# Kernel optimization log

Hardware: AMD Instinct MI355X
Metric: run time of the kernel (lower is better)

Reference implementation:

```python
import jax, jax.numpy as jnp
import numpy as np

B, M, V, D = 2048, 2, 25, 64      # batch, max_body, joints, input channels
C1, C2, K, U = 128, 256, 3, 256   # gcn hidden, gcn out, A kernel size, lstm units
NJ, NB = M * V * U, M * U         # joint / body state widths
SD = NJ + NB + U                  # full state dim = 13568


def _hs(z):
    # keras hard_sigmoid
    return jnp.clip(0.2 * z + 0.5, 0.0, 1.0)


def _lstm_step(z, c):
    i = _hs(z[..., :U])
    f = _hs(z[..., U:2 * U])
    g = jnp.tanh(z[..., 2 * U:3 * U])
    o = _hs(z[..., 3 * U:])
    c2 = f * c + i * g
    return o * jnp.tanh(c2), c2


def _forget_bias(shape_prefix):
    z = jnp.zeros(shape_prefix + (U,), jnp.float32)
    return jnp.concatenate([z, jnp.ones_like(z), z, z], axis=-1)


def setup_inputs() -> dict:
    key = jax.random.key(0)
    ks = jax.random.split(key, 16)
    f = lambda i, shape, s: jax.random.normal(ks[i], shape, jnp.float32) * s
    x = f(0, (B, M * V * D), 1.0)
    h0 = f(1, (B, SD), 0.1)
    c0 = f(2, (B, SD), 0.1)
    A = jax.random.uniform(ks[3], (K, V, V), jnp.float32)
    A = A / jnp.sum(A, axis=-1, keepdims=True)  # row-normalized adjacency stack
    edge_importance = jnp.ones((2, K, V, V), jnp.float32)
    return dict(
        x=x, h0=h0, c0=c0, A=A, edge_importance=edge_importance,
        wg0=f(4, (D, C1 * K), 0.05), bg0=jnp.zeros((C1 * K,), jnp.float32),
        wg1=f(5, (C1, C2 * K), 0.05), bg1=jnp.zeros((C2 * K,), jnp.float32),
        wr1=f(6, (C1, C2), 0.05), br1=jnp.zeros((C2,), jnp.float32),
        kernel=f(7, (C2, 4 * U), 0.02),
        kernel_body=f(8, (V * C2, 4 * U), 0.01),
        kernel_whole=f(9, (M * V * C2, 4 * U), 0.005),
        rk=f(10, (U, 4 * U), 0.02),
        rk_body=f(11, (U, 4 * U), 0.02),
        rk_whole=f(12, (U, 4 * U), 0.02),
        bias=_forget_bias((M, V)),
        bias_body=_forget_bias((M,)),
        bias_whole=_forget_bias((1,)),
    )


def reference(x, h0, c0, A, edge_importance, wg0, bg0, wg1, bg1, wr1, br1,
              kernel, kernel_body, kernel_whole, rk, rk_body, rk_whole,
              bias, bias_body, bias_whole):
    N = B * M
    xg = x.reshape(N, V, D)
    # --- GCN layer 0: 1x1 conv -> split K -> edge-weighted adjacency einsum ---
    y = (xg @ wg0 + bg0).reshape(N, V, K, C1)
    y = jnp.einsum('nvkc,kvw->nwc', y, edge_importance[0] * A)
    y = jax.nn.relu(y)
    # --- GCN layer 1 (channels change -> residual 1x1 conv) ---
    res = y @ wr1 + br1
    z = (y @ wg1 + bg1).reshape(N, V, K, C2)
    z = jnp.einsum('nvkc,kvw->nwc', z, edge_importance[1] * A) + res
    feat = jax.nn.relu(z).reshape(B, M, V, C2)
    # --- unpack multi-scale state ---
    h_j = h0[:, :NJ].reshape(B, M, V, U)
    c_j = c0[:, :NJ].reshape(B, M, V, U)
    h_b = h0[:, NJ:NJ + NB].reshape(B, M, U)
    c_b = c0[:, NJ:NJ + NB].reshape(B, M, U)
    h_w = h0[:, NJ + NB:]
    c_w = c0[:, NJ + NB:]
    # --- joint-scale gates ---
    zj = jnp.einsum('bmvc,cu->bmvu', feat, kernel) + h_j @ rk + bias
    h_j2, c_j2 = _lstm_step(zj, c_j)
    # --- body-scale gates ---
    zb = feat.reshape(B, M, V * C2) @ kernel_body + h_b @ rk_body + bias_body
    h_b2, c_b2 = _lstm_step(zb, c_b)
    # --- whole-scale gates ---
    zw = feat.reshape(B, M * V * C2) @ kernel_whole + h_w @ rk_whole + bias_whole[0]
    h_w2, c_w2 = _lstm_step(zw, c_w)
    h_new = jnp.concatenate([h_j2.reshape(B, NJ), h_b2.reshape(B, NB), h_w2], axis=-1)
    return h_new
```

## Files before the change

kernel.cpp:

```cpp
#include <hip/hip_runtime.h>
#include <hip/hip_bf16.h>
#include <math.h>

constexpr int Bn = 2048, Mm = 2, Vv = 25, Dd = 64;
constexpr int C1 = 128, C2 = 256, Kk = 3, Uu = 256;
constexpr int NJ = Mm*Vv*Uu;
constexpr int NBd = Mm*Uu;
constexpr int SD = NJ+NBd+Uu;
constexpr int Nn = Bn*Mm;
constexpr int N3 = Nn*Vv;
constexpr int NCH = 2;
constexpr int NnC = Nn/NCH;
constexpr int RCn = NnC*Vv;

typedef __bf16 v8bf __attribute__((ext_vector_type(8)));
typedef float f32x16 __attribute__((ext_vector_type(16)));

__device__ __forceinline__ float hsig(float z){ return fminf(fmaxf(0.2f*z+0.5f,0.f),1.f); }
__device__ __forceinline__ float ftanh(float x){
  float e = __expf(2.f*x);
  return 1.f - 2.f*__frcp_rn(e+1.f);
}
__device__ __forceinline__ unsigned short f2bs(float x){
  __hip_bfloat16 h = __float2bfloat16(x);
  unsigned short s; __builtin_memcpy(&s, &h, 2); return s;
}
__device__ __forceinline__ float bs2f(unsigned short s){
  unsigned u = ((unsigned)s)<<16; float f; __builtin_memcpy(&f,&u,4); return f;
}

#if defined(__has_builtin)
#if __has_builtin(__builtin_amdgcn_global_load_lds)
#define HAS_ALD 1
#endif
#endif
#ifndef HAS_ALD
#define HAS_ALD 0
#endif
__device__ __forceinline__ void stage16(unsigned short* dst_base, int lane, const void* src){
#if HAS_ALD
  __builtin_amdgcn_global_load_lds(
      (const __attribute__((address_space(1))) unsigned int*)src,
      (__attribute__((address_space(3))) unsigned int*)dst_base, 16, 0, 0);
#else
  *(uint4*)(dst_base + lane*8) = *(const uint4*)src;
#endif
}

template<int SW, typename TI>
__global__ __launch_bounds__(SW*3) void kMix(
    const TI* __restrict__ src, const float* __restrict__ Amat,
    const float* __restrict__ ei, int eoff, unsigned short* __restrict__ dst)
{
  __shared__ float xs[Vv*SW];
  __shared__ float as[Kk*Vv*Vv];
  const int n = blockIdx.x, t = threadIdx.x;
  const TI* srow = src + (size_t)n*(Vv*SW);
  for(int i=t;i<Vv*SW;i+=SW*3){
    if constexpr (sizeof(TI)==2) xs[i]=bs2f((unsigned short)srow[i]);
    else xs[i]=srow[i];
  }
  for(int i=t;i<Kk*Vv*Vv;i+=SW*3) as[i]=ei[eoff+i]*Amat[i];
  __syncthreads();
  const int k = t/SW, d = t%SW;
  float acc[Vv];
  #pragma unroll
  for(int w=0;w<Vv;++w) acc[w]=0.f;
  for(int v=0;v<Vv;++v){
    float xv = xs[v*SW+d];
    const float* ap = &as[k*625 + v*25];
    #pragma unroll
    for(int w=0;w<Vv;++w) acc[w] += ap[w]*xv;
  }
  unsigned short* drow = dst + (size_t)n*(Vv*3*SW);
  for(int w=0;w<Vv;++w) drow[w*(3*SW) + t] = f2bs(acc[w]);
}

template<int MODE>
__device__ __forceinline__ size_t hoffOf(int row){
  if constexpr (MODE==0){ int b=row/50, j=row-b*50; return (size_t)b*SD + j*256; }
  else if constexpr (MODE==1){ int b=row>>1, m=row&1; return (size_t)b*SD + NJ + m*256; }
  else return (size_t)row*SD + NJ + NBd;
}

template<int MODE>
__global__ __launch_bounds__(256) void kConvW(
    const float* __restrict__ Wm, const float* __restrict__ Wr,
    unsigned short* __restrict__ out, int total)
{
  int i = blockIdx.x*256 + threadIdx.x;
  if(i>=total) return;
  int e = i&7, ln = (i>>3)&63, l31 = ln&31, l5 = ln>>5;
  float v;
  if constexpr (MODE<=2){
    constexpr int KF = (MODE==0)?256:(MODE==1)?6400:12800;
    constexpr int NKT = (KF+256)/32;
    int fb = (i>>9)&15, kt = (i>>13)%NKT, ublk = i/(NKT*8192);
    int kh = fb&1, cg = fb>>1;
    int k = kt*32 + l5*8 + kh*16 + e;
    int g = cg&3, uu = (cg>>2)*32 + l31;
    int col = g*256 + ublk*64 + uu;
    v = (k<KF) ? Wm[(size_t)k*1024+col] : Wr[(size_t)(k-KF)*1024+col];
  } else if constexpr (MODE==3){
    int fb = (i>>9)&15, kt = i>>13;
    int kh = fb&1, cg = fb>>1;
    int k = kt*32 + l5*8 + kh*16 + e;
    int col = cg*32 + l31;
    v = (k<384) ? Wm[(size_t)(k&127)*768 + (k>>7)*256 + col]
                : Wr[(size_t)(k-384)*256 + col];
  } else {
    int fb = (i>>9)&7, kt = i>>12;
    int kh = fb&1, cg = fb>>1;
    int k = kt*32 + l5*8 + kh*16 + e;
    int col = cg*32 + l31;
    v = Wm[(size_t)(k&63)*384 + (k>>6)*128 + col];
  }
  out[i] = f2bs(v);
}

template<int MODE>
__global__ __launch_bounds__(256) void kConvH(
    const float* __restrict__ h0, unsigned short* __restrict__ dst, int total4)
{
  int i = blockIdx.x*256 + threadIdx.x;
  if(i>=total4) return;
  int row = i>>6, k4 = (i&63)*4;
  const float* s = h0 + hoffOf<MODE>(row) + k4;
  float4 f = *(const float4*)s;
  uint2 o;
  o.x = (unsigned)f2bs(f.x) | ((unsigned)f2bs(f.y)<<16);
  o.y = (unsigned)f2bs(f.z) | ((unsigned)f2bs(f.w)<<16);
  *(uint2*)(dst + (size_t)i*4) = o;
}

template<int MODE>
__global__ __launch_bounds__(512,2) void kLSTMm(
    const unsigned short* __restrict__ featb, const unsigned short* __restrict__ h0b,
    const float* __restrict__ c0, const unsigned short* __restrict__ Wcat,
    const float* __restrict__ bias, float* __restrict__ outp, int KC)
{
  constexpr int KF = (MODE==0)?256:(MODE==1)?6400:12800;
  constexpr int KT = KF+256;
  constexpr int NKT = KT/32;
  constexpr int ROWS = (MODE==0)?N3:(MODE==1)?Nn:Bn;
  __shared__ unsigned short Afr[2][8*512];
  __shared__ unsigned short Bfr[2][16*512];
  const int t = threadIdx.x;
  const int bx = blockIdx.x;
  const int r0 = (bx>>2)*128;
  const int ublk = bx&3;
  const int z = (MODE==0)?0:blockIdx.y;
  const int kBeg = z*KC, kEnd = min(KT, kBeg+KC);
  const int lane = t&63, wid = t>>6;
  const int wr = wid>>1, w2 = wid&1;
  const int l31 = lane&31, l5 = lane>>5;

  f32x16 acc[4];
  #pragma unroll
  for(int g=0;g<4;++g)
    #pragma unroll
    for(int j=0;j<16;++j) acc[g][j]=0.f;

  auto stageA = [&](unsigned short* dstb, int k0){
    int row = r0 + (wid>>1)*32 + l31;
    int kg = k0 + ((wid&1)*2 + l5)*8;
    const unsigned short* src = (kg < KF)
        ? featb + (size_t)row*KF + kg
        : h0b   + (size_t)row*256 + (kg - KF);
    stage16(dstb + (size_t)(wid*64)*8, lane, src);
  };
  auto stageB = [&](unsigned short* dstb, int k0){
    const unsigned short* wt = Wcat + ((size_t)ublk*NKT + (k0>>5))*8192;
    #pragma unroll
    for(int i=0;i<2;++i){
      int off = i*512 + wid*64;
      stage16(dstb + (size_t)off*8, lane, wt + (size_t)(off + lane)*8);
    }
  };

  stageA(Afr[0], kBeg); stageB(Bfr[0], kBeg);
  __syncthreads();
  const int nst = (kEnd-kBeg)>>5;
  for(int s=0; s<nst; ++s){
    const int cur = s&1;
    if(s+1<nst){ stageA(Afr[cur^1], kBeg+(s+1)*32); stageB(Bfr[cur^1], kBeg+(s+1)*32); }
    #pragma unroll
    for(int kh=0; kh<2; ++kh){
      v8bf a = *(const v8bf*)&Afr[cur][((wr*2+kh)*512 + lane*8)];
      #pragma unroll
      for(int g=0; g<4; ++g){
        v8bf b = *(const v8bf*)&Bfr[cur][((w2*4+g)*2+kh)*512 + lane*8];
        acc[g] = __builtin_amdgcn_mfma_f32_32x32x16_bf16(a, b, acc[g], 0, 0, 0);
      }
    }
    __syncthreads();
  }

  const int u = ublk*64 + w2*32 + l31;
  if constexpr (MODE==0){
    #pragma unroll
    for(int reg=0; reg<16; ++reg){
      int row = r0 + wr*32 + (reg&3) + 8*(reg>>2) + 4*l5;
      int b = row/50, j = row - b*50;
      size_t hoff = (size_t)b*SD + j*256;
      int boff = j*1024;
      float zi = acc[0][reg] + bias[boff + u];
      float zf = acc[1][reg] + bias[boff + 256 + u];
      float zg = acc[2][reg] + bias[boff + 512 + u];
      float zo = acc[3][reg] + bias[boff + 768 + u];
      float iv=hsig(zi), fv=hsig(zf), gv=ftanh(zg), ov=hsig(zo);
      float cc = c0[hoff+u];
      float c2 = fv*cc + iv*gv;
      outp[hoff+u] = ov*ftanh(c2);
    }
  } else {
    #pragma unroll
    for(int reg=0; reg<16; ++reg){
      int row = r0 + wr*32 + (reg&3) + 8*(reg>>2) + 4*l5;
      float* base = outp + ((size_t)z*ROWS + row)*1024 + u;
      base[0]   = acc[0][reg];
      base[256] = acc[1][reg];
      base[512] = acc[2][reg];
      base[768] = acc[3][reg];
    }
  }
}

__global__ __launch_bounds__(512,2) void kGC2(
    const unsigned short* __restrict__ ycat, const unsigned short* __restrict__ yb,
    const unsigned short* __restrict__ Wc2, const float* __restrict__ bg1,
    const float* __restrict__ br1, const float* __restrict__ Amat,
    const float* __restrict__ ei, unsigned short* __restrict__ featb)
{
  __shared__ unsigned short Afr[2][8*512];
  __shared__ unsigned short Bfr[2][16*512];
  __shared__ float asums[75];
  const int t = threadIdx.x;
  const int r0 = blockIdx.x*128;
  if(t<75){
    int k=t/25, w=t%25; float s=0.f;
    for(int v=0;v<25;++v) s += ei[1875 + k*625+v*25+w]*Amat[k*625+v*25+w];
    asums[t]=s;
  }
  const int lane = t&63, wid = t>>6;
  const int wr = wid>>1, w2 = wid&1;
  const int l31 = lane&31, l5 = lane>>5;
  f32x16 acc[4];
  #pragma unroll
  for(int g=0;g<4;++g)
    #pragma unroll
    for(int j=0;j<16;++j) acc[g][j]=0.f;

  auto stageA = [&](unsigned short* dst, int k0){
    int row = r0 + (wid>>1)*32 + l31;
    int kg = k0 + ((wid&1)*2 + l5)*8;
    const unsigned short* src = (kg<384) ? ycat + (size_t)row*384 + kg
                                         : yb   + (size_t)row*128 + (kg-384);
    stage16(dst + (size_t)(wid*64)*8, lane, src);
  };
  auto stageB = [&](unsigned short* dst, int k0){
    const unsigned short* wt = Wc2 + (size_t)(k0>>5)*8192;
    #pragma unroll
    for(int i=0;i<2;++i){
      int off = i*512 + wid*64;
      stage16(dst + (size_t)off*8, lane, wt + (size_t)(off + lane)*8);
    }
  };

  stageA(Afr[0],0); stageB(Bfr[0],0);
  __syncthreads();
  for(int s=0; s<16; ++s){
    const int cur = s&1;
    if(s+1<16){ stageA(Afr[cur^1],(s+1)*32); stageB(Bfr[cur^1],(s+1)*32); }
    #pragma unroll
    for(int kh=0; kh<2; ++kh){
      v8bf a = *(const v8bf*)&Afr[cur][(wr*2+kh)*512 + lane*8];
      #pragma unroll
      for(int g=0; g<4; ++g){
        v8bf b = *(const v8bf*)&Bfr[cur][((w2*4+g)*2+kh)*512 + lane*8];
        acc[g] = __builtin_amdgcn_mfma_f32_32x32x16_bf16(a, b, acc[g], 0, 0, 0);
      }
    }
    __syncthreads();
  }
  #pragma unroll
  for(int reg=0; reg<16; ++reg){
    int row = r0 + wr*32 + (reg&3) + 8*(reg>>2) + 4*l5;
    int w = row % 25;
    float a0w = asums[w], a1w = asums[25+w], a2w = asums[50+w];
    #pragma unroll
    for(int g=0; g<4; ++g){
      int cc = w2*128 + g*32 + l31;
      float b = br1[cc] + a0w*bg1[cc] + a1w*bg1[256+cc] + a2w*bg1[512+cc];
      featb[(size_t)row*256 + cc] = f2bs(fmaxf(acc[g][reg] + b, 0.f));
    }
  }
}

__global__ __launch_bounds__(512,2) void kGC1(
    const unsigned short* __restrict__ xcat, const unsigned short* __restrict__ Wc1,
    const float* __restrict__ bg0, const float* __restrict__ Amat,
    const float* __restrict__ ei, unsigned short* __restrict__ yb)
{
  __shared__ unsigned short Afr[2][8*512];
  __shared__ unsigned short Bfr[2][8*512];
  __shared__ float asums[75];
  const int t = threadIdx.x;
  const int r0 = blockIdx.x*128;
  if(t<75){
    int k=t/25, w=t%25; float s=0.f;
    for(int v=0;v<25;++v) s += ei[k*625+v*25+w]*Amat[k*625+v*25+w];
    asums[t]=s;
  }
  const int lane = t&63, wid = t>>6;
  const int wr = wid>>1, w2 = wid&1;
  const int l31 = lane&31, l5 = lane>>5;
  f32x16 acc[2];
  #pragma unroll
  for(int g=0;g<2;++g)
    #pragma unroll
    for(int j=0;j<16;++j) acc[g][j]=0.f;

  auto stageA = [&](unsigned short* dst, int k0){
    int row = r0 + (wid>>1)*32 + l31;
    int kg = k0 + ((wid&1)*2 + l5)*8;
    stage16(dst + (size_t)(wid*64)*8, lane, xcat + (size_t)row*192 + kg);
  };
  auto stageB = [&](unsigned short* dst, int k0){
    const unsigned short* wt = Wc1 + (size_t)(k0>>5)*4096;
    int off = wid*64;
    stage16(dst + (size_t)off*8, lane, wt + (size_t)(off + lane)*8);
  };

  stageA(Afr[0],0); stageB(Bfr[0],0);
  __syncthreads();
  for(int s=0; s<6; ++s){
    const int cur = s&1;
    if(s+1<6){ stageA(Afr[cur^1],(s+1)*32); stageB(Bfr[cur^1],(s+1)*32); }
    #pragma unroll
    for(int kh=0; kh<2; ++kh){
      v8bf a = *(const v8bf*)&Afr[cur][(wr*2+kh)*512 + lane*8];
      #pragma unroll
      for(int g=0; g<2; ++g){
        v8bf b = *(const v8bf*)&Bfr[cur][((w2*2+g)*2+kh)*512 + lane*8];
        acc[g] = __builtin_amdgcn_mfma_f32_32x32x16_bf16(a, b, acc[g], 0, 0, 0);
      }
    }
    __syncthreads();
  }
  #pragma unroll
  for(int reg=0; reg<16; ++reg){
    int row = r0 + wr*32 + (reg&3) + 8*(reg>>2) + 4*l5;
    int w = row % 25;
    float a0w = asums[w], a1w = asums[25+w], a2w = asums[50+w];
    #pragma unroll
    for(int g=0; g<2; ++g){
      int cc = w2*64 + g*32 + l31;
      float b = a0w*bg0[cc] + a1w*bg0[128+cc] + a2w*bg0[256+cc];
      yb[(size_t)row*128 + cc] = f2bs(fmaxf(acc[g][reg] + b, 0.f));
    }
  }
}

template<int MODE>
__global__ __launch_bounds__(256) void kFin(
    const float* __restrict__ part, const float* __restrict__ c0,
    const float* __restrict__ bias, float* __restrict__ out, int S)
{
  constexpr int ROWS = (MODE==1)?Nn:Bn;
  const int row = blockIdx.x, u = threadIdx.x;
  size_t hoff = hoffOf<MODE>(row);
  int boff = (MODE==1)?((row&1)*1024):0;
  float zg4[4] = { bias[boff+u], bias[boff+256+u], bias[boff+512+u], bias[boff+768+u] };
  for(int s=0;s<S;++s){
    const float* p = part + ((size_t)s*ROWS + row)*1024;
    #pragma unroll
    for(int g=0;g<4;++g) zg4[g] += p[g*256+u];
  }
  float iv=hsig(zg4[0]), fv=hsig(zg4[1]), gv=ftanh(zg4[2]), ov=hsig(zg4[3]);
  float cc = c0[hoff+u];
  float c2 = fv*cc + iv*gv;
  out[hoff+u] = ov*ftanh(c2);
}

extern "C" void kernel_launch(void* const* d_in, const int* in_sizes, int n_in,
                              void* d_out, int out_size, void* d_ws, size_t ws_size,
                              hipStream_t stream)
{
  const float* x   = (const float*)d_in[0];
  const float* h0  = (const float*)d_in[1];
  const float* c0  = (const float*)d_in[2];
  const float* A   = (const float*)d_in[3];
  const float* ei  = (const float*)d_in[4];
  const float* wg0 = (const float*)d_in[5];
  const float* bg0 = (const float*)d_in[6];
  const float* wg1 = (const float*)d_in[7];
  const float* bg1 = (const float*)d_in[8];
  const float* wr1 = (const float*)d_in[9];
  const float* br1 = (const float*)d_in[10];
  const float* kern  = (const float*)d_in[11];
  const float* kernB = (const float*)d_in[12];
  const float* kernW = (const float*)d_in[13];
  const float* rk    = (const float*)d_in[14];
  const float* rkB   = (const float*)d_in[15];
  const float* rkW   = (const float*)d_in[16];
  const float* bias  = (const float*)d_in[17];
  const float* biasB = (const float*)d_in[18];
  const float* biasW = (const float*)d_in[19];
  float* out = (float*)d_out;
  char* wsb  = (char*)d_ws;

  unsigned short* featb = (unsigned short*)wsb;
  unsigned short* WbJ = (unsigned short*)(wsb + 52428800);
  unsigned short* WbB = WbJ + 524288;
  unsigned short* WbW = WbB + 6815744;
  unsigned short* Wc2 = WbW + 13369344;
  unsigned short* Wc1 = Wc2 + 131072;
  char* dyn = wsb + 94158848;
  unsigned short* ycat = (unsigned short*)dyn;
  unsigned short* xcat = ycat;
  unsigned short* yb   = (unsigned short*)(dyn + 39321600);
  unsigned short* h0bJ = (unsigned short*)dyn;
  float* part = (float*)dyn;
  unsigned short* hB = (unsigned short*)(wsb + 146587648);
  unsigned short* hW = hB + 1048576;

  kConvW<0><<<(524288+255)/256,   256, 0, stream>>>(kern,  rk,  WbJ, 524288);
  kConvW<1><<<(6815744+255)/256,  256, 0, stream>>>(kernB, rkB, WbB, 6815744);
  kConvW<2><<<(13369344+255)/256, 256, 0, stream>>>(kernW, rkW, WbW, 13369344);
  kConvW<3><<<(131072+255)/256,   256, 0, stream>>>(wg1, wr1, Wc2, 131072);
  kConvW<4><<<(24576+255)/256,    256, 0, stream>>>(wg0, nullptr, Wc1, 24576);
  kConvH<1><<<(262144+255)/256, 256, 0, stream>>>(h0, hB, 262144);
  kConvH<2><<<(131072+255)/256, 256, 0, stream>>>(h0, hW, 131072);

  for(int c=0;c<NCH;++c){
    const float* xc = x + (size_t)c*NnC*(Vv*Dd);
    kMix<64,float>          <<<NnC, 192, 0, stream>>>(xc, A, ei, 0, xcat);
    kGC1<<<RCn/128, 512, 0, stream>>>(xcat, Wc1, bg0, A, ei, yb);
    kMix<128,unsigned short><<<NnC, 384, 0, stream>>>(yb, A, ei, 1875, ycat);
    kGC2<<<RCn/128, 512, 0, stream>>>(ycat, yb, Wc2, bg1, br1, A, ei,
                                      featb + (size_t)c*RCn*256);
  }
  kConvH<0><<<(6553600+255)/256, 256, 0, stream>>>(h0, h0bJ, 6553600);
  kLSTMm<0><<<(N3/128)*4, 512, 0, stream>>>(featb, h0bJ, c0, WbJ, bias, out, 512);
  kLSTMm<1><<<dim3((Nn/128)*4,3), 512, 0, stream>>>(featb, hB, nullptr, WbB, nullptr, part, 2240);
  kFin<1><<<Nn, 256, 0, stream>>>(part, c0, biasB, out, 3);
  kLSTMm<2><<<dim3((Bn/128)*4,6), 512, 0, stream>>>(featb, hW, nullptr, WbW, nullptr, part, 2176);
  kFin<2><<<Bn, 256, 0, stream>>>(part, c0, biasW, out, 6);
}
```

Measured before the change: 701.0 us.

## Triple-buffer LDS staging with vmcnt-based waits in GEMM kernels

Moves the LSTM and both GCN GEMM kernels from double-buffered to triple-buffered LDS tiles. Each loop iteration now waits on an explicit vmcnt counter and raw s_barrier instead of a full __syncthreads drain, so two tiles of global-to-LDS loads stay in flight while MFMA runs on the oldest one. The extra buffer raises LDS use per block, which may limit occupancy. Correctness depends on stage16 issuing exactly the assumed number of async loads per stage.

```diff
diff --git a/kernel.cpp b/kernel.cpp
--- a/kernel.cpp
+++ b/kernel.cpp
@@ -143,8 +143,8 @@
   constexpr int KT = KF+256;
   constexpr int NKT = KT/32;
   constexpr int ROWS = (MODE==0)?N3:(MODE==1)?Nn:Bn;
-  __shared__ unsigned short Afr[2][8*512];
-  __shared__ unsigned short Bfr[2][16*512];
+  __shared__ unsigned short Afr[3][8*512];
+  __shared__ unsigned short Bfr[3][16*512];
   const int t = threadIdx.x;
   const int bx = blockIdx.x;
   const int r0 = (bx>>2)*128;
@@ -177,24 +177,34 @@
       stage16(dstb + (size_t)off*8, lane, wt + (size_t)(off + lane)*8);
     }
   };
-
-  stageA(Afr[0], kBeg); stageB(Bfr[0], kBeg);
-  __syncthreads();
-  const int nst = (kEnd-kBeg)>>5;
-  for(int s=0; s<nst; ++s){
-    const int cur = s&1;
-    if(s+1<nst){ stageA(Afr[cur^1], kBeg+(s+1)*32); stageB(Bfr[cur^1], kBeg+(s+1)*32); }
+  auto mstep = [&](const unsigned short* Ab, const unsigned short* Bb){
     #pragma unroll
     for(int kh=0; kh<2; ++kh){
-      v8bf a = *(const v8bf*)&Afr[cur][((wr*2+kh)*512 + lane*8)];
+      v8bf a = *(const v8bf*)&Ab[(wr*2+kh)*512 + lane*8];
       #pragma unroll
       for(int g=0; g<4; ++g){
-        v8bf b = *(const v8bf*)&Bfr[cur][((w2*4+g)*2+kh)*512 + lane*8];
+        v8bf b = *(const v8bf*)&Bb[((w2*4+g)*2+kh)*512 + lane*8];
         acc[g] = __builtin_amdgcn_mfma_f32_32x32x16_bf16(a, b, acc[g], 0, 0, 0);
       }
     }
-    __syncthreads();
-  }
+  };
+
+  unsigned short *A0=&Afr[0][0], *A1=&Afr[1][0], *A2=&Afr[2][0];
+  unsigned short *B0=&Bfr[0][0], *B1=&Bfr[1][0], *B2=&Bfr[2][0];
+  const int nst = (kEnd-kBeg)>>5;
+  stageA(A0, kBeg);    stageB(B0, kBeg);
+  stageA(A1, kBeg+32); stageB(B1, kBeg+32);
+  for(int s=0; s<nst-1; ++s){
+    asm volatile("s_waitcnt vmcnt(3)" ::: "memory");
+    __builtin_amdgcn_s_barrier();
+    if(s+2<nst){ stageA(A2, kBeg+(s+2)*32); stageB(B2, kBeg+(s+2)*32); }
+    mstep(A0, B0);
+    unsigned short* ta=A0; A0=A1; A1=A2; A2=ta;
+    unsigned short* tb=B0; B0=B1; B1=B2; B2=tb;
+  }
+  asm volatile("s_waitcnt vmcnt(0)" ::: "memory");
+  __builtin_amdgcn_s_barrier();
+  mstep(A0, B0);
 
   const int u = ublk*64 + w2*32 + l31;
   if constexpr (MODE==0){
@@ -232,8 +242,8 @@
     const float* __restrict__ br1, const float* __restrict__ Amat,
     const float* __restrict__ ei, unsigned short* __restrict__ featb)
 {
-  __shared__ unsigned short Afr[2][8*512];
-  __shared__ unsigned short Bfr[2][16*512];
+  __shared__ unsigned short Afr[3][8*512];
+  __shared__ unsigned short Bfr[3][16*512];
   __shared__ float asums[75];
   const int t = threadIdx.x;
   const int r0 = blockIdx.x*128;
@@ -266,23 +276,34 @@
       stage16(dst + (size_t)off*8, lane, wt + (size_t)(off + lane)*8);
     }
   };
-
-  stageA(Afr[0],0); stageB(Bfr[0],0);
-  __syncthreads();
-  for(int s=0; s<16; ++s){
-    const int cur = s&1;
-    if(s+1<16){ stageA(Afr[cur^1],(s+1)*32); stageB(Bfr[cur^1],(s+1)*32); }
+  auto mstep = [&](const unsigned short* Ab, const unsigned short* Bb){
     #pragma unroll
     for(int kh=0; kh<2; ++kh){
-      v8bf a = *(const v8bf*)&Afr[cur][(wr*2+kh)*512 + lane*8];
+      v8bf a = *(const v8bf*)&Ab[(wr*2+kh)*512 + lane*8];
       #pragma unroll
       for(int g=0; g<4; ++g){
-        v8bf b = *(const v8bf*)&Bfr[cur][((w2*4+g)*2+kh)*512 + lane*8];
+        v8bf b = *(const v8bf*)&Bb[((w2*4+g)*2+kh)*512 + lane*8];
         acc[g] = __builtin_amdgcn_mfma_f32_32x32x16_bf16(a, b, acc[g], 0, 0, 0);
       }
     }
-    __syncthreads();
-  }
+  };
+
+  unsigned short *A0=&Afr[0][0], *A1=&Afr[1][0], *A2=&Afr[2][0];
+  unsigned short *B0=&Bfr[0][0], *B1=&Bfr[1][0], *B2=&Bfr[2][0];
+  stageA(A0,0);  stageB(B0,0);
+  stageA(A1,32); stageB(B1,32);
+  for(int s=0; s<15; ++s){
+    asm volatile("s_waitcnt vmcnt(3)" ::: "memory");
+    __builtin_amdgcn_s_barrier();
+    if(s+2<16){ stageA(A2,(s+2)*32); stageB(B2,(s+2)*32); }
+    mstep(A0,B0);
+    unsigned short* ta=A0; A0=A1; A1=A2; A2=ta;
+    unsigned short* tb=B0; B0=B1; B1=B2; B2=tb;
+  }
+  asm volatile("s_waitcnt vmcnt(0)" ::: "memory");
+  __builtin_amdgcn_s_barrier();
+  mstep(A0,B0);
+
   #pragma unroll
   for(int reg=0; reg<16; ++reg){
     int row = r0 + wr*32 + (reg&3) + 8*(reg>>2) + 4*l5;
@@ -302,8 +323,8 @@
     const float* __restrict__ bg0, const float* __restrict__ Amat,
     const float* __restrict__ ei, unsigned short* __restrict__ yb)
 {
-  __shared__ unsigned short Afr[2][8*512];
-  __shared__ unsigned short Bfr[2][8*512];
+  __shared__ unsigned short Afr[3][8*512];
+  __shared__ unsigned short Bfr[3][8*512];
   __shared__ float asums[75];
   const int t = threadIdx.x;
   const int r0 = blockIdx.x*128;
@@ -331,23 +352,34 @@
     int off = wid*64;
     stage16(dst + (size_t)off*8, lane, wt + (size_t)(off + lane)*8);
   };
-
-  stageA(Afr[0],0); stageB(Bfr[0],0);
-  __syncthreads();
-  for(int s=0; s<6; ++s){
-    const int cur = s&1;
-    if(s+1<6){ stageA(Afr[cur^1],(s+1)*32); stageB(Bfr[cur^1],(s+1)*32); }
+  auto mstep = [&](const unsigned short* Ab, const unsigned short* Bb){
     #pragma unroll
     for(int kh=0; kh<2; ++kh){
-      v8bf a = *(const v8bf*)&Afr[cur][(wr*2+kh)*512 + lane*8];
+      v8bf a = *(const v8bf*)&Ab[(wr*2+kh)*512 + lane*8];
       #pragma unroll
       for(int g=0; g<2; ++g){
-        v8bf b = *(const v8bf*)&Bfr[cur][((w2*2+g)*2+kh)*512 + lane*8];
+        v8bf b = *(const v8bf*)&Bb[((w2*2+g)*2+kh)*512 + lane*8];
         acc[g] = __builtin_amdgcn_mfma_f32_32x32x16_bf16(a, b, acc[g], 0, 0, 0);
       }
     }
-    __syncthreads();
-  }
+  };
+
+  unsigned short *A0=&Afr[0][0], *A1=&Afr[1][0], *A2=&Afr[2][0];
+  unsigned short *B0=&Bfr[0][0], *B1=&Bfr[1][0], *B2=&Bfr[2][0];
+  stageA(A0,0);  stageB(B0,0);
+  stageA(A1,32); stageB(B1,32);
+  for(int s=0; s<5; ++s){
+    asm volatile("s_waitcnt vmcnt(2)" ::: "memory");
+    __builtin_amdgcn_s_barrier();
+    if(s+2<6){ stageA(A2,(s+2)*32); stageB(B2,(s+2)*32); }
+    mstep(A0,B0);
+    unsigned short* ta=A0; A0=A1; A1=A2; A2=ta;
+    unsigned short* tb=B0; B0=B1; B1=B2; B2=tb;
+  }
+  asm volatile("s_waitcnt vmcnt(0)" ::: "memory");
+  __builtin_amdgcn_s_barrier();
+  mstep(A0,B0);
+
   #pragma unroll
   for(int reg=0; reg<16; ++reg){
     int row = r0 + wr*32 + (reg&3) + 8*(reg>>2) + 4*l5;
```

After: 691.1 us. No clear change (-1.4%).
